# Kernel optimization log

Measured on AMD Instinct MI355X. Metric: run time of the kernel, lower is better.

## Reference

```python
import jax, jax.numpy as jnp
import numpy as np

N, IN, OUT, R, E = 20000, 768, 768, 8, 320000


def setup_inputs() -> dict:
    key = jax.random.key(0)
    ks = jax.random.split(key, 9)
    x = jax.random.normal(ks[0], (N, IN), dtype=jnp.float32)
    edge_index = jax.random.randint(ks[1], (2, E), 0, N, dtype=jnp.int64)
    edge_type = jax.random.randint(ks[2], (E,), 0, R, dtype=jnp.int64)
    s1 = 1.0 / np.sqrt(IN)
    s2 = 1.0 / np.sqrt(OUT)
    W1 = jax.random.normal(ks[3], (R, IN, OUT), dtype=jnp.float32) * s1
    root1 = jax.random.normal(ks[4], (IN, OUT), dtype=jnp.float32) * s1
    b1 = jnp.zeros((OUT,), dtype=jnp.float32)
    W2 = jax.random.normal(ks[5], (R, OUT, OUT), dtype=jnp.float32) * s2
    root2 = jax.random.normal(ks[6], (OUT, OUT), dtype=jnp.float32) * s2
    b2 = jnp.zeros((OUT,), dtype=jnp.float32)
    return {"x": x, "edge_index": edge_index, "edge_type": edge_type,
            "W1": W1, "root1": root1, "b1": b1,
            "W2": W2, "root2": root2, "b2": b2}


def _rgcn_conv(x, src, dst, etype, W, root, b):
    # PyG RGCNConv: per-relation mean aggregation of neighbor features,
    # then relation-specific linear transform, plus root weight and bias.
    # mean(x_j @ W_r) == mean(x_j) @ W_r, so aggregate first, transform after.
    num_nodes = x.shape[0]
    num_rel = W.shape[0]
    x_src = x[src]                                  # [E, d_in]
    seg = dst * num_rel + etype                     # composite (node, relation) id
    sums = jax.ops.segment_sum(x_src, seg, num_segments=num_nodes * num_rel)
    cnt = jax.ops.segment_sum(jnp.ones((src.shape[0],), dtype=x.dtype), seg,
                              num_segments=num_nodes * num_rel)
    mean = sums / jnp.maximum(cnt, 1.0)[:, None]    # [N*R, d_in]
    mean = mean.reshape(num_nodes, num_rel, -1)     # [N, R, d_in]
    out = jnp.einsum('nri,rio->no', mean, W)        # relation-batched matmul
    return out + x @ root + b


def reference(x, edge_index, edge_type, W1, root1, b1, W2, root2, b2):
    src, dst = edge_index[0], edge_index[1]
    h = _rgcn_conv(x, src, dst, edge_type, W1, root1, b1)
    h = jax.nn.relu(h)
    out = _rgcn_conv(h, src, dst, edge_type, W2, root2, b2)
    return out
```

## Files before the change

kernel.cpp:

```cpp
#include <hip/hip_runtime.h>
#include <hip/hip_bf16.h>
#include <stdint.h>

#define N_NODES 20000
#define DIM     768
#define NREL    8
#define NEDGE   320000
#define NSEG    (N_NODES * NREL)
#define GKA     6144
#define GK      6912
#define NPW     2

typedef short short8 __attribute__((ext_vector_type(8)));
typedef float f32x4  __attribute__((ext_vector_type(4)));

__device__ __forceinline__ void async_load16(const void* g, void* l) {
  __builtin_amdgcn_global_load_lds((const __attribute__((address_space(1))) void*)g,
                                   (__attribute__((address_space(3))) void*)l,
                                   16, 0, 0);
}

__device__ __forceinline__ float bf_lo(uint32_t v) {
  return __builtin_bit_cast(float, v << 16);
}
__device__ __forceinline__ float bf_hi(uint32_t v) {
  return __builtin_bit_cast(float, v & 0xffff0000u);
}
__device__ __forceinline__ uint32_t pack_bf16x2(float a, float b) {
  uint32_t lo = __builtin_bit_cast(unsigned short, __float2bfloat16(a));
  uint32_t hi = __builtin_bit_cast(unsigned short, __float2bfloat16(b));
  return lo | (hi << 16);
}

__global__ void seg_count_kernel(const int* __restrict__ dst, const int* __restrict__ et,
                                 int* __restrict__ segcnt, int e_cnt) {
  int e = blockIdx.x * 256 + threadIdx.x;
  if (e < e_cnt) atomicAdd(&segcnt[dst[e] * NREL + et[e]], 1);
}

__global__ void block_scan_kernel(const int* __restrict__ in, int* __restrict__ out,
                                  int* __restrict__ partials, int n) {
  __shared__ int wsum[16];
  const int t = threadIdx.x, lane = t & 63, wave = t >> 6;
  const int i = blockIdx.x * 1024 + t;
  int v = (i < n) ? in[i] : 0;
  int s = v;
#pragma unroll
  for (int off = 1; off < 64; off <<= 1) {
    int u = __shfl_up(s, off, 64);
    if (lane >= off) s += u;
  }
  if (lane == 63) wsum[wave] = s;
  __syncthreads();
  if (t < 16) {
    int w = wsum[t];
#pragma unroll
    for (int off = 1; off < 16; off <<= 1) {
      int u = __shfl_up(w, off, 64);
      if (t >= off) w += u;
    }
    wsum[t] = w;
  }
  __syncthreads();
  const int basew = (wave > 0) ? wsum[wave - 1] : 0;
  if (i < n) out[i] = basew + s - v;
  if (t == 1023) partials[blockIdx.x] = wsum[15];
}

__global__ void partial_scan_kernel(int* __restrict__ partials, int nb) {
  const int lane = threadIdx.x & 63;
  int carry = 0;
  for (int base = 0; base < nb; base += 64) {
    const int i = base + lane;
    int v = (i < nb) ? partials[i] : 0;
    int s = v;
#pragma unroll
    for (int off = 1; off < 64; off <<= 1) {
      int u = __shfl_up(s, off, 64);
      if (lane >= off) s += u;
    }
    if (i < nb) partials[i] = carry + s - v;
    carry += __shfl(s, 63, 64);
  }
}

__global__ void add_offsets_kernel(int* __restrict__ soffs, const int* __restrict__ partials,
                                   int* __restrict__ cursor, int n) {
  const int i = blockIdx.x * 1024 + threadIdx.x;
  if (i < n) {
    const int v = soffs[i] + partials[blockIdx.x];
    soffs[i] = v;
    cursor[i] = v;
  }
  if (i == 0) soffs[n] = NEDGE;
}

__global__ void seg_scatter_kernel(const int* __restrict__ src, const int* __restrict__ dst,
                                   const int* __restrict__ et, int* __restrict__ cursor,
                                   int* __restrict__ es, int e_cnt) {
  int e = blockIdx.x * 256 + threadIdx.x;
  if (e < e_cnt) {
    const int seg = dst[e] * NREL + et[e];
    const int p = atomicAdd(&cursor[seg], 1);
    es[p] = src[e];
  }
}

__global__ void cvt_bf16_kernel(const float4* __restrict__ in, ushort4* __restrict__ out, int n4) {
  int i = blockIdx.x * 256 + threadIdx.x;
  if (i < n4) {
    float4 f = in[i];
    ushort4 r;
    r.x = __builtin_bit_cast(unsigned short, __float2bfloat16(f.x));
    r.y = __builtin_bit_cast(unsigned short, __float2bfloat16(f.y));
    r.z = __builtin_bit_cast(unsigned short, __float2bfloat16(f.z));
    r.w = __builtin_bit_cast(unsigned short, __float2bfloat16(f.w));
    out[i] = r;
  }
}

__global__ void transpose_w_kernel(const float* __restrict__ src, __hip_bfloat16* __restrict__ dst,
                                   int rows, int col_off) {
  __shared__ float tile[32][33];
  const int c0 = blockIdx.x * 32;
  const int r0 = blockIdx.y * 32;
  const int tx = threadIdx.x, ty = threadIdx.y;
  for (int i = ty; i < 32; i += 8) {
    int r = r0 + i, c = c0 + tx;
    tile[i][tx] = (r < rows) ? src[(size_t)r * DIM + c] : 0.f;
  }
  __syncthreads();
  for (int i = ty; i < 32; i += 8) {
    int c = c0 + i, r = r0 + tx;
    if (r < rows)
      dst[(size_t)c * GK + col_off + r] = __float2bfloat16(tile[tx][i]);
  }
}

__global__ __launch_bounds__(256) void aggregate_kernel(
    const __hip_bfloat16* __restrict__ feat,
    const int* __restrict__ soffs, const int* __restrict__ es,
    __hip_bfloat16* __restrict__ Abuf,
    int node_base, int rows) {
  const int t = threadIdx.x;
  const int lane = t & 63;
  const int wave = t >> 6;
  const int boff = lane * 8;

  int nloc = (blockIdx.x * 4 + wave) * NPW;
  for (int it = 0; it < NPW; ++it, ++nloc) {
    if (nloc >= rows) return;
    const int n = node_base + nloc;
    char* Ab = (char*)(Abuf + (size_t)nloc * GKA);
#pragma unroll
    for (int r = 0; r < NREL; ++r) {
      const int beg = soffs[n * NREL + r], end = soffs[n * NREL + r + 1];
      float acc[12];
#pragma unroll
      for (int i = 0; i < 12; ++i) acc[i] = 0.f;
      int e = beg;
      for (; e + 2 <= end; e += 2) {
        const int s0 = es[e], s1 = es[e + 1];
        const char* p0 = (const char*)(feat + (size_t)s0 * DIM) + boff;
        const char* p1 = (const char*)(feat + (size_t)s1 * DIM) + boff;
        const uint2 a0 = *(const uint2*)(p0);
        const uint2 a1 = *(const uint2*)(p0 + 512);
        const uint2 a2 = *(const uint2*)(p0 + 1024);
        const uint2 b0 = *(const uint2*)(p1);
        const uint2 b1 = *(const uint2*)(p1 + 512);
        const uint2 b2 = *(const uint2*)(p1 + 1024);
        acc[0]  += bf_lo(a0.x); acc[1]  += bf_hi(a0.x);
        acc[2]  += bf_lo(a0.y); acc[3]  += bf_hi(a0.y);
        acc[4]  += bf_lo(a1.x); acc[5]  += bf_hi(a1.x);
        acc[6]  += bf_lo(a1.y); acc[7]  += bf_hi(a1.y);
        acc[8]  += bf_lo(a2.x); acc[9]  += bf_hi(a2.x);
        acc[10] += bf_lo(a2.y); acc[11] += bf_hi(a2.y);
        acc[0]  += bf_lo(b0.x); acc[1]  += bf_hi(b0.x);
        acc[2]  += bf_lo(b0.y); acc[3]  += bf_hi(b0.y);
        acc[4]  += bf_lo(b1.x); acc[5]  += bf_hi(b1.x);
        acc[6]  += bf_lo(b1.y); acc[7]  += bf_hi(b1.y);
        acc[8]  += bf_lo(b2.x); acc[9]  += bf_hi(b2.x);
        acc[10] += bf_lo(b2.y); acc[11] += bf_hi(b2.y);
      }
      if (e < end) {
        const int s0 = es[e];
        const char* p0 = (const char*)(feat + (size_t)s0 * DIM) + boff;
        const uint2 a0 = *(const uint2*)(p0);
        const uint2 a1 = *(const uint2*)(p0 + 512);
        const uint2 a2 = *(const uint2*)(p0 + 1024);
        acc[0]  += bf_lo(a0.x); acc[1]  += bf_hi(a0.x);
        acc[2]  += bf_lo(a0.y); acc[3]  += bf_hi(a0.y);
        acc[4]  += bf_lo(a1.x); acc[5]  += bf_hi(a1.x);
        acc[6]  += bf_lo(a1.y); acc[7]  += bf_hi(a1.y);
        acc[8]  += bf_lo(a2.x); acc[9]  += bf_hi(a2.x);
        acc[10] += bf_lo(a2.y); acc[11] += bf_hi(a2.y);
      }
      const float inv = 1.f / fmaxf((float)(end - beg), 1.f);
      uint2 o0, o1, o2;
      o0.x = pack_bf16x2(acc[0] * inv, acc[1] * inv);
      o0.y = pack_bf16x2(acc[2] * inv, acc[3] * inv);
      o1.x = pack_bf16x2(acc[4] * inv, acc[5] * inv);
      o1.y = pack_bf16x2(acc[6] * inv, acc[7] * inv);
      o2.x = pack_bf16x2(acc[8] * inv, acc[9] * inv);
      o2.y = pack_bf16x2(acc[10] * inv, acc[11] * inv);
      char* dst = Ab + r * (DIM * 2);
      *(uint2*)(dst + boff) = o0;
      *(uint2*)(dst + boff + 512) = o1;
      *(uint2*)(dst + boff + 1024) = o2;
    }
  }
}

__global__ __launch_bounds__(256, 3) void gemm_kernel(
    const __hip_bfloat16* __restrict__ A,
    const __hip_bfloat16* __restrict__ feat,
    const __hip_bfloat16* __restrict__ BT,
    const float* __restrict__ bias,
    __hip_bfloat16* __restrict__ outb,
    float* __restrict__ outf,
    int mvalid, int node_base, int mode) {
  __shared__ __hip_bfloat16 Asm[128][64];
  __shared__ __hip_bfloat16 Bsm[128][64];
  const int t = threadIdx.x;
  const int lane = t & 63;
  const int wave = t >> 6;
  const int m0 = blockIdx.y * 128;
  const int n0 = blockIdx.x * 128;

  const int srow = lane >> 3;
  const int sg = (lane & 7) ^ srow;
  const int arow = m0 + wave * 32 + srow;
  const __hip_bfloat16* ag = A  + (size_t)arow * GKA + sg * 8;
  const __hip_bfloat16* fg = feat + (size_t)(node_base + arow) * DIM + sg * 8;
  const __hip_bfloat16* bg = BT + (size_t)(n0 + wave * 32 + srow) * GK + sg * 8;

  f32x4 acc[4][4] = {};
  const int wm = (wave >> 1) * 64;
  const int wn = (wave & 1) * 64;
  const int ml = lane & 15;
  const int quad = lane >> 4;
  const int sw = ml & 7;

#define KSTEP(APTR, ASTRIDE)                                                       \
  {                                                                                \
    __syncthreads();                                                               \
    _Pragma("unroll")                                                              \
    for (int ib = 0; ib < 4; ++ib)                                                 \
      async_load16(APTR + (size_t)ib * 8 * (ASTRIDE), &Asm[wave * 32 + ib * 8][0]);\
    _Pragma("unroll")                                                              \
    for (int ib = 0; ib < 4; ++ib)                                                 \
      async_load16(bg + (size_t)ib * 8 * GK, &Bsm[wave * 32 + ib * 8][0]);         \
    bg += 64;                                                                      \
    __syncthreads();                                                               \
    _Pragma("unroll")                                                              \
    for (int ks = 0; ks < 2; ++ks) {                                               \
      const int go = (((ks * 4 + quad) ^ sw) * 8);                                 \
      short8 a[4], b[4];                                                           \
      _Pragma("unroll")                                                            \
      for (int i = 0; i < 4; ++i) a[i] = *(const short8*)&Asm[wm + i * 16 + ml][go];\
      _Pragma("unroll")                                                            \
      for (int i = 0; i < 4; ++i) b[i] = *(const short8*)&Bsm[wn + i * 16 + ml][go];\
      _Pragma("unroll")                                                            \
      for (int i = 0; i < 4; ++i)                                                  \
        _Pragma("unroll")                                                          \
        for (int j = 0; j < 4; ++j)                                                \
          acc[i][j] = __builtin_amdgcn_mfma_f32_16x16x32_bf16(a[i], b[j], acc[i][j], 0, 0, 0); \
    }                                                                              \
  }

  for (int kt = 0; kt < GKA / 64; ++kt) {
    KSTEP(ag, GKA);
    ag += 64;
  }
  for (int kt = 0; kt < DIM / 64; ++kt) {
    KSTEP(fg, DIM);
    fg += 64;
  }
#undef KSTEP

  float bcol[4];
#pragma unroll
  for (int nt = 0; nt < 4; ++nt) bcol[nt] = bias[n0 + wn + nt * 16 + ml];
#pragma unroll
  for (int mt = 0; mt < 4; ++mt) {
#pragma unroll
    for (int rr = 0; rr < 4; ++rr) {
      int row = m0 + wm + mt * 16 + quad * 4 + rr;
      if (row < mvalid) {
        size_t orow = (size_t)(node_base + row) * DIM;
#pragma unroll
        for (int nt = 0; nt < 4; ++nt) {
          int col = n0 + wn + nt * 16 + ml;
          float v = acc[mt][nt][rr] + bcol[nt];
          if (mode == 0) outb[orow + col] = __float2bfloat16(fmaxf(v, 0.f));
          else           outf[orow + col] = v;
        }
      }
    }
  }
}

extern "C" void kernel_launch(void* const* d_in, const int* in_sizes, int n_in,
                              void* d_out, int out_size, void* d_ws, size_t ws_size,
                              hipStream_t stream) {
  const float* x     = (const float*)d_in[0];
  const int*   eidx  = (const int*)d_in[1];
  const int*   etype = (const int*)d_in[2];
  const float* W1    = (const float*)d_in[3];
  const float* root1 = (const float*)d_in[4];
  const float* b1    = (const float*)d_in[5];
  const float* W2    = (const float*)d_in[6];
  const float* root2 = (const float*)d_in[7];
  const float* b2    = (const float*)d_in[8];
  float* out = (float*)d_out;
  const int* esrc_in = eidx;
  const int* edst_in = eidx + NEDGE;

  char* p = (char*)d_ws;
  auto alloc = [&](size_t bytes) -> char* {
    char* r = p;
    p += (bytes + 255) & ~(size_t)255;
    return r;
  };
  __hip_bfloat16* xb  = (__hip_bfloat16*)alloc((size_t)N_NODES * DIM * 2);
  __hip_bfloat16* hb  = (__hip_bfloat16*)alloc((size_t)N_NODES * DIM * 2);
  __hip_bfloat16* w1t = (__hip_bfloat16*)alloc((size_t)DIM * GK * 2);
  __hip_bfloat16* w2t = (__hip_bfloat16*)alloc((size_t)DIM * GK * 2);
  int* segcnt   = (int*)alloc((size_t)NSEG * 4);
  int* soffs    = (int*)alloc((size_t)(NSEG + 1) * 4);
  int* cursor   = (int*)alloc((size_t)NSEG * 4);
  int* partials = (int*)alloc(256 * 4);
  int* es       = (int*)alloc((size_t)NEDGE * 4);
  size_t used = (size_t)(p - (char*)d_ws);
  size_t remain = (ws_size > used) ? (ws_size - used) : 0;
  long long caprows_ll = (long long)(remain / ((size_t)GKA * 2));
  int caprows = (int)((caprows_ll / 128) * 128);
  if (caprows > 20096) caprows = 20096;
  if (caprows < 128) caprows = 128;
  __hip_bfloat16* Abuf = (__hip_bfloat16*)p;

  const int NB = (NSEG + 1023) / 1024;
  hipMemsetAsync(segcnt, 0, (size_t)NSEG * 4, stream);
  seg_count_kernel<<<(NEDGE + 255) / 256, 256, 0, stream>>>(edst_in, etype, segcnt, NEDGE);
  block_scan_kernel<<<NB, 1024, 0, stream>>>(segcnt, soffs, partials, NSEG);
  partial_scan_kernel<<<1, 64, 0, stream>>>(partials, NB);
  add_offsets_kernel<<<NB, 1024, 0, stream>>>(soffs, partials, cursor, NSEG);
  seg_scatter_kernel<<<(NEDGE + 255) / 256, 256, 0, stream>>>(esrc_in, edst_in, etype, cursor, es, NEDGE);

  cvt_bf16_kernel<<<((N_NODES * DIM / 4) + 255) / 256, 256, 0, stream>>>(
      (const float4*)x, (ushort4*)xb, N_NODES * DIM / 4);
  dim3 tb(32, 8);
  transpose_w_kernel<<<dim3(DIM / 32, (NREL * DIM) / 32), tb, 0, stream>>>(W1, w1t, NREL * DIM, 0);
  transpose_w_kernel<<<dim3(DIM / 32, DIM / 32), tb, 0, stream>>>(root1, w1t, DIM, NREL * DIM);
  transpose_w_kernel<<<dim3(DIM / 32, (NREL * DIM) / 32), tb, 0, stream>>>(W2, w2t, NREL * DIM, 0);
  transpose_w_kernel<<<dim3(DIM / 32, DIM / 32), tb, 0, stream>>>(root2, w2t, DIM, NREL * DIM);

  for (int base = 0; base < N_NODES; base += caprows) {
    int rows = N_NODES - base; if (rows > caprows) rows = caprows;
    int agrid = (rows + 4 * NPW - 1) / (4 * NPW);
    aggregate_kernel<<<agrid, 256, 0, stream>>>(xb, soffs, es, Abuf, base, rows);
    dim3 grid(DIM / 128, (rows + 127) / 128);
    gemm_kernel<<<grid, 256, 0, stream>>>(Abuf, xb, w1t, b1, hb, nullptr, rows, base, 0);
  }
  for (int base = 0; base < N_NODES; base += caprows) {
    int rows = N_NODES - base; if (rows > caprows) rows = caprows;
    int agrid = (rows + 4 * NPW - 1) / (4 * NPW);
    aggregate_kernel<<<agrid, 256, 0, stream>>>(hb, soffs, es, Abuf, base, rows);
    dim3 grid(DIM / 128, (rows + 127) / 128);
    gemm_kernel<<<grid, 256, 0, stream>>>(Abuf, hb, w2t, b2, nullptr, out, rows, base, 1);
  }
}
```

Baseline: 1.111 ms.

## Widen GEMM tile to 128x256 with 512 threads and unroll aggregation by four

The GEMM moves to a 128x256 output tile computed by 8 waves sharing one LDS buffer, and it merges the aggregated-A and root-feature K loops into a single loop that switches source pointer partway through. The wider tile halves the number of A-tile reloads across the N dimension and gives more MFMA work per barrier. The aggregation kernel now issues four edge gathers before accumulating, to keep more loads in flight, and stops unrolling the relation loop. The trade-off is higher register and LDS pressure per block, fewer blocks in the grid, and a launch-bounds hint of 4 blocks per CU that may not be attainable.

```diff
diff --git a/kernel.cpp b/kernel.cpp
--- a/kernel.cpp
+++ b/kernel.cpp
@@ -152,66 +152,59 @@
     if (nloc >= rows) return;
     const int n = node_base + nloc;
     char* Ab = (char*)(Abuf + (size_t)nloc * GKA);
-#pragma unroll
+#pragma unroll 1
     for (int r = 0; r < NREL; ++r) {
       const int beg = soffs[n * NREL + r], end = soffs[n * NREL + r + 1];
       float acc[12];
 #pragma unroll
       for (int i = 0; i < 12; ++i) acc[i] = 0.f;
       int e = beg;
-      for (; e + 2 <= end; e += 2) {
-        const int s0 = es[e], s1 = es[e + 1];
-        const char* p0 = (const char*)(feat + (size_t)s0 * DIM) + boff;
-        const char* p1 = (const char*)(feat + (size_t)s1 * DIM) + boff;
-        const uint2 a0 = *(const uint2*)(p0);
-        const uint2 a1 = *(const uint2*)(p0 + 512);
-        const uint2 a2 = *(const uint2*)(p0 + 1024);
-        const uint2 b0 = *(const uint2*)(p1);
-        const uint2 b1 = *(const uint2*)(p1 + 512);
-        const uint2 b2 = *(const uint2*)(p1 + 1024);
-        acc[0]  += bf_lo(a0.x); acc[1]  += bf_hi(a0.x);
-        acc[2]  += bf_lo(a0.y); acc[3]  += bf_hi(a0.y);
-        acc[4]  += bf_lo(a1.x); acc[5]  += bf_hi(a1.x);
-        acc[6]  += bf_lo(a1.y); acc[7]  += bf_hi(a1.y);
-        acc[8]  += bf_lo(a2.x); acc[9]  += bf_hi(a2.x);
-        acc[10] += bf_lo(a2.y); acc[11] += bf_hi(a2.y);
-        acc[0]  += bf_lo(b0.x); acc[1]  += bf_hi(b0.x);
-        acc[2]  += bf_lo(b0.y); acc[3]  += bf_hi(b0.y);
-        acc[4]  += bf_lo(b1.x); acc[5]  += bf_hi(b1.x);
-        acc[6]  += bf_lo(b1.y); acc[7]  += bf_hi(b1.y);
-        acc[8]  += bf_lo(b2.x); acc[9]  += bf_hi(b2.x);
-        acc[10] += bf_lo(b2.y); acc[11] += bf_hi(b2.y);
+      for (; e + 4 <= end; e += 4) {
+        uint2 v[4][3];
+#pragma unroll
+        for (int j = 0; j < 4; ++j) {
+          const char* pp = (const char*)(feat + (size_t)es[e + j] * DIM) + boff;
+          v[j][0] = *(const uint2*)(pp);
+          v[j][1] = *(const uint2*)(pp + 512);
+          v[j][2] = *(const uint2*)(pp + 1024);
+        }
+#pragma unroll
+        for (int j = 0; j < 4; ++j) {
+#pragma unroll
+          for (int q = 0; q < 3; ++q) {
+            acc[4 * q + 0] += bf_lo(v[j][q].x);
+            acc[4 * q + 1] += bf_hi(v[j][q].x);
+            acc[4 * q + 2] += bf_lo(v[j][q].y);
+            acc[4 * q + 3] += bf_hi(v[j][q].y);
+          }
+        }
       }
-      if (e < end) {
-        const int s0 = es[e];
-        const char* p0 = (const char*)(feat + (size_t)s0 * DIM) + boff;
-        const uint2 a0 = *(const uint2*)(p0);
-        const uint2 a1 = *(const uint2*)(p0 + 512);
-        const uint2 a2 = *(const uint2*)(p0 + 1024);
-        acc[0]  += bf_lo(a0.x); acc[1]  += bf_hi(a0.x);
-        acc[2]  += bf_lo(a0.y); acc[3]  += bf_hi(a0.y);
-        acc[4]  += bf_lo(a1.x); acc[5]  += bf_hi(a1.x);
-        acc[6]  += bf_lo(a1.y); acc[7]  += bf_hi(a1.y);
-        acc[8]  += bf_lo(a2.x); acc[9]  += bf_hi(a2.x);
-        acc[10] += bf_lo(a2.y); acc[11] += bf_hi(a2.y);
+      for (; e < end; ++e) {
+        const char* pp = (const char*)(feat + (size_t)es[e] * DIM) + boff;
+        uint2 a0 = *(const uint2*)(pp);
+        uint2 a1 = *(const uint2*)(pp + 512);
+        uint2 a2 = *(const uint2*)(pp + 1024);
+        acc[0] += bf_lo(a0.x); acc[1] += bf_hi(a0.x); acc[2]  += bf_lo(a0.y); acc[3]  += bf_hi(a0.y);
+        acc[4] += bf_lo(a1.x); acc[5] += bf_hi(a1.x); acc[6]  += bf_lo(a1.y); acc[7]  += bf_hi(a1.y);
+        acc[8] += bf_lo(a2.x); acc[9] += bf_hi(a2.x); acc[10] += bf_lo(a2.y); acc[11] += bf_hi(a2.y);
       }
       const float inv = 1.f / fmaxf((float)(end - beg), 1.f);
-      uint2 o0, o1, o2;
-      o0.x = pack_bf16x2(acc[0] * inv, acc[1] * inv);
-      o0.y = pack_bf16x2(acc[2] * inv, acc[3] * inv);
-      o1.x = pack_bf16x2(acc[4] * inv, acc[5] * inv);
-      o1.y = pack_bf16x2(acc[6] * inv, acc[7] * inv);
-      o2.x = pack_bf16x2(acc[8] * inv, acc[9] * inv);
-      o2.y = pack_bf16x2(acc[10] * inv, acc[11] * inv);
       char* dst = Ab + r * (DIM * 2);
-      *(uint2*)(dst + boff) = o0;
-      *(uint2*)(dst + boff + 512) = o1;
-      *(uint2*)(dst + boff + 1024) = o2;
-    }
-  }
-}
-
-__global__ __launch_bounds__(256, 3) void gemm_kernel(
+      uint2 o;
+      o.x = pack_bf16x2(acc[0] * inv, acc[1] * inv);
+      o.y = pack_bf16x2(acc[2] * inv, acc[3] * inv);
+      *(uint2*)(dst + boff) = o;
+      o.x = pack_bf16x2(acc[4] * inv, acc[5] * inv);
+      o.y = pack_bf16x2(acc[6] * inv, acc[7] * inv);
+      *(uint2*)(dst + boff + 512) = o;
+      o.x = pack_bf16x2(acc[8] * inv, acc[9] * inv);
+      o.y = pack_bf16x2(acc[10] * inv, acc[11] * inv);
+      *(uint2*)(dst + boff + 1024) = o;
+    }
+  }
+}
+
+__global__ __launch_bounds__(512, 4) void gemm_kernel(
     const __hip_bfloat16* __restrict__ A,
     const __hip_bfloat16* __restrict__ feat,
     const __hip_bfloat16* __restrict__ BT,
@@ -219,64 +212,62 @@
     __hip_bfloat16* __restrict__ outb,
     float* __restrict__ outf,
     int mvalid, int node_base, int mode) {
-  __shared__ __hip_bfloat16 Asm[128][64];
-  __shared__ __hip_bfloat16 Bsm[128][64];
+  __shared__ __hip_bfloat16 Sm[384 * 64];
   const int t = threadIdx.x;
   const int lane = t & 63;
   const int wave = t >> 6;
   const int m0 = blockIdx.y * 128;
-  const int n0 = blockIdx.x * 128;
+  const int n0 = blockIdx.x * 256;
 
   const int srow = lane >> 3;
   const int sg = (lane & 7) ^ srow;
-  const int arow = m0 + wave * 32 + srow;
-  const __hip_bfloat16* ag = A  + (size_t)arow * GKA + sg * 8;
-  const __hip_bfloat16* fg = feat + (size_t)(node_base + arow) * DIM + sg * 8;
-  const __hip_bfloat16* bg = BT + (size_t)(n0 + wave * 32 + srow) * GK + sg * 8;
+  const int crow0 = wave * 48;
+  const __hip_bfloat16* gsrc[6];
+#pragma unroll
+  for (int ib = 0; ib < 6; ++ib) {
+    const int rb = crow0 + ib * 8;
+    if (rb < 128) gsrc[ib] = A + (size_t)(m0 + rb + srow) * GKA + sg * 8;
+    else          gsrc[ib] = BT + (size_t)(n0 + rb - 128 + srow) * GK + sg * 8;
+  }
 
   f32x4 acc[4][4] = {};
-  const int wm = (wave >> 1) * 64;
-  const int wn = (wave & 1) * 64;
+  const int wm = (wave >> 2) * 64;
+  const int wn = (wave & 3) * 64;
   const int ml = lane & 15;
   const int quad = lane >> 4;
   const int sw = ml & 7;
 
-#define KSTEP(APTR, ASTRIDE)                                                       \
-  {                                                                                \
-    __syncthreads();                                                               \
-    _Pragma("unroll")                                                              \
-    for (int ib = 0; ib < 4; ++ib)                                                 \
-      async_load16(APTR + (size_t)ib * 8 * (ASTRIDE), &Asm[wave * 32 + ib * 8][0]);\
-    _Pragma("unroll")                                                              \
-    for (int ib = 0; ib < 4; ++ib)                                                 \
-      async_load16(bg + (size_t)ib * 8 * GK, &Bsm[wave * 32 + ib * 8][0]);         \
-    bg += 64;                                                                      \
-    __syncthreads();                                                               \
-    _Pragma("unroll")                                                              \
-    for (int ks = 0; ks < 2; ++ks) {                                               \
-      const int go = (((ks * 4 + quad) ^ sw) * 8);                                 \
-      short8 a[4], b[4];                                                           \
-      _Pragma("unroll")                                                            \
-      for (int i = 0; i < 4; ++i) a[i] = *(const short8*)&Asm[wm + i * 16 + ml][go];\
-      _Pragma("unroll")                                                            \
-      for (int i = 0; i < 4; ++i) b[i] = *(const short8*)&Bsm[wn + i * 16 + ml][go];\
-      _Pragma("unroll")                                                            \
-      for (int i = 0; i < 4; ++i)                                                  \
-        _Pragma("unroll")                                                          \
-        for (int j = 0; j < 4; ++j)                                                \
-          acc[i][j] = __builtin_amdgcn_mfma_f32_16x16x32_bf16(a[i], b[j], acc[i][j], 0, 0, 0); \
-    }                                                                              \
-  }
-
-  for (int kt = 0; kt < GKA / 64; ++kt) {
-    KSTEP(ag, GKA);
-    ag += 64;
-  }
-  for (int kt = 0; kt < DIM / 64; ++kt) {
-    KSTEP(fg, DIM);
-    fg += 64;
-  }
-#undef KSTEP
+  for (int kt = 0; kt < GK / 64; ++kt) {
+    __syncthreads();
+    if (kt == GKA / 64) {
+#pragma unroll
+      for (int ib = 0; ib < 6; ++ib) {
+        const int rb = crow0 + ib * 8;
+        if (rb < 128)
+          gsrc[ib] = feat + (size_t)(node_base + m0 + rb + srow) * DIM + sg * 8;
+      }
+    }
+#pragma unroll
+    for (int ib = 0; ib < 6; ++ib) {
+      async_load16(gsrc[ib], &Sm[(crow0 + ib * 8) * 64]);
+      gsrc[ib] += 64;
+    }
+    __syncthreads();
+#pragma unroll
+    for (int ks = 0; ks < 2; ++ks) {
+      const int go = (((ks * 4 + quad) ^ sw) * 8);
+      short8 a[4], b[4];
+#pragma unroll
+      for (int i = 0; i < 4; ++i) a[i] = *(const short8*)&Sm[(wm + i * 16 + ml) * 64 + go];
+#pragma unroll
+      for (int j = 0; j < 4; ++j) b[j] = *(const short8*)&Sm[(128 + wn + j * 16 + ml) * 64 + go];
+#pragma unroll
+      for (int i = 0; i < 4; ++i)
+#pragma unroll
+        for (int j = 0; j < 4; ++j)
+          acc[i][j] = __builtin_amdgcn_mfma_f32_16x16x32_bf16(a[i], b[j], acc[i][j], 0, 0, 0);
+    }
+  }
 
   float bcol[4];
 #pragma unroll
@@ -359,14 +350,14 @@
     int rows = N_NODES - base; if (rows > caprows) rows = caprows;
     int agrid = (rows + 4 * NPW - 1) / (4 * NPW);
     aggregate_kernel<<<agrid, 256, 0, stream>>>(xb, soffs, es, Abuf, base, rows);
-    dim3 grid(DIM / 128, (rows + 127) / 128);
-    gemm_kernel<<<grid, 256, 0, stream>>>(Abuf, xb, w1t, b1, hb, nullptr, rows, base, 0);
+    dim3 grid(DIM / 256, (rows + 127) / 128);
+    gemm_kernel<<<grid, 512, 0, stream>>>(Abuf, xb, w1t, b1, hb, nullptr, rows, base, 0);
   }
   for (int base = 0; base < N_NODES; base += caprows) {
     int rows = N_NODES - base; if (rows > caprows) rows = caprows;
     int agrid = (rows + 4 * NPW - 1) / (4 * NPW);
     aggregate_kernel<<<agrid, 256, 0, stream>>>(hb, soffs, es, Abuf, base, rows);
-    dim3 grid(DIM / 128, (rows + 127) / 128);
-    gemm_kernel<<<grid, 256, 0, stream>>>(Abuf, hb, w2t, b2, nullptr, out, rows, base, 1);
-  }
-}
+    dim3 grid(DIM / 256, (rows + 127) / 128);
+    gemm_kernel<<<grid, 512, 0, stream>>>(Abuf, hb, w2t, b2, nullptr, out, rows, base, 1);
+  }
+}
```

New measurement: 1.202 ms. 1.08x slower.
